# Performance work log

Hardware: AMD Instinct MI355X
Metric: run time of the kernel (lower is better)

Reference implementation:

```python
import jax, jax.numpy as jnp
import numpy as np

BN_EPS = 1e-5


def _bn(y, g, b, m, v):
    # BatchNorm1d in eval mode (running stats), faithful to torch's affine BN
    return (y - m) * jax.lax.rsqrt(v + BN_EPS) * g + b


def setup_inputs() -> dict:
    key = jax.random.key(0)
    ks = jax.random.split(key, 6)
    N, E, C_IN, C_OUT = 20000, 640000, 128, 256
    x = jax.random.normal(ks[0], (N, C_IN), dtype=jnp.float32)
    tpl_edge_index = jax.random.randint(ks[1], (2, E), 0, N, dtype=jnp.int64)
    def lin(k, o, i):
        return jax.random.normal(k, (o, i), dtype=jnp.float32) * 0.05
    inp = {
        'x': x,
        'tpl_edge_index': tpl_edge_index,
        'W1': lin(ks[2], C_OUT, 2 * C_IN), 'b1': jnp.zeros((C_OUT,), jnp.float32),
        'g1': jnp.ones((C_OUT,), jnp.float32), 'be1': jnp.zeros((C_OUT,), jnp.float32),
        'm1': jnp.zeros((C_OUT,), jnp.float32), 'v1': jnp.ones((C_OUT,), jnp.float32),
        'W2': lin(ks[3], C_OUT, C_OUT), 'b2': jnp.zeros((C_OUT,), jnp.float32),
        'g2': jnp.ones((C_OUT,), jnp.float32), 'be2': jnp.zeros((C_OUT,), jnp.float32),
        'm2': jnp.zeros((C_OUT,), jnp.float32), 'v2': jnp.ones((C_OUT,), jnp.float32),
        'W3': lin(ks[4], C_OUT, C_OUT), 'b3': jnp.zeros((C_OUT,), jnp.float32),
        'g3': jnp.ones((C_OUT,), jnp.float32), 'be3': jnp.zeros((C_OUT,), jnp.float32),
        'm3': jnp.zeros((C_OUT,), jnp.float32), 'v3': jnp.ones((C_OUT,), jnp.float32),
    }
    return inp


def reference(x, tpl_edge_index, W1, b1, g1, be1, m1, v1,
              W2, b2, g2, be2, m2, v2, W3, b3, g3, be3, m3, v3):
    N = x.shape[0]
    # remove_self_loops + add_self_loops: under max aggregation, duplicate
    # self-loop messages (x_j - x_i == 0) are idempotent, so appending one
    # self-loop per node is mathematically identical.
    loops = jnp.arange(N, dtype=tpl_edge_index.dtype)
    src = jnp.concatenate([tpl_edge_index[0], loops])  # x_j indices
    tgt = jnp.concatenate([tpl_edge_index[1], loops])  # x_i / aggregation indices
    x_i = x[tgt]                                       # [E+N, C_in]
    x_j = x[src]
    h = jnp.concatenate([x_i, x_j - x_i], axis=1)      # [E+N, 2*C_in]
    h = _bn(jax.nn.relu(h @ W1.T + b1), g1, be1, m1, v1)
    h = _bn(jax.nn.relu(h @ W2.T + b2), g2, be2, m2, v2)
    agg = jax.ops.segment_max(h, tgt, num_segments=N)  # scatter-max -> [N, C_out]
    out = _bn(jax.nn.relu(agg @ W3.T + b3), g3, be3, m3, v3)
    return out
```

## Files before the change

kernel.cpp:

```cpp
#include <hip/hip_runtime.h>
#include <stdint.h>

#define BN_EPS 1e-5f

typedef __bf16 bf16x8 __attribute__((ext_vector_type(8)));
typedef __bf16 bf16x2 __attribute__((ext_vector_type(2)));
typedef float  f32x4  __attribute__((ext_vector_type(4)));
typedef float  f32x2  __attribute__((ext_vector_type(2)));

__device__ __forceinline__ unsigned short f2bf(float f) {
    unsigned u = __float_as_uint(f);
    unsigned r = (u + 0x7FFFu + ((u >> 16) & 1u)) >> 16;
    return (unsigned short)r;
}
__device__ __forceinline__ unsigned pkb(float a, float b) {
    f32x2 f; f.x = a; f.y = b;
    bf16x2 h = __builtin_convertvector(f, bf16x2);
    return *(unsigned*)&h;
}
__device__ __forceinline__ unsigned ar2(unsigned p, unsigned q) {
    f32x2 a, b;
    a.x = __uint_as_float(p << 16);
    a.y = __uint_as_float(p & 0xFFFF0000u);
    b.x = __uint_as_float(q << 16);
    b.y = __uint_as_float(q & 0xFFFF0000u);
    f32x2 s = a + b;
    return pkb(fmaxf(s.x, 0.f), fmaxf(s.y, 0.f));
}
__device__ __forceinline__ int swz(int row, int k) {
    const int blk = k >> 3;
    const int sb = (blk & 24) | ((blk ^ row) & 7);
    return (row << 8) + (sb << 3) + (k & 7);
}
__device__ __forceinline__ int swz128(int row, int k) {
    const int blk = k >> 3;
    const int sb = (blk & 8) | ((blk ^ row) & 7);
    return (row << 7) + (sb << 3) + (k & 7);
}

__global__ void prep_kernel(
    const float* __restrict__ x, const int* __restrict__ eidx,
    int E, int M, int NX,
    const float* __restrict__ W1, const float* __restrict__ W2, const float* __restrict__ W3,
    const float* __restrict__ b1, const float* __restrict__ g1, const float* __restrict__ be1,
    const float* __restrict__ m1, const float* __restrict__ v1,
    const float* __restrict__ b2, const float* __restrict__ g2, const float* __restrict__ be2,
    const float* __restrict__ m2, const float* __restrict__ v2,
    const float* __restrict__ b3, const float* __restrict__ g3, const float* __restrict__ be3,
    const float* __restrict__ m3, const float* __restrict__ v3,
    unsigned short* __restrict__ W1b, unsigned short* __restrict__ W2b,
    unsigned short* __restrict__ W3b, float* __restrict__ consts,
    unsigned* __restrict__ mask2,
    unsigned short* __restrict__ xb, unsigned* __restrict__ count)
{
    const int idx = blockIdx.x * 256 + threadIdx.x;
    if (idx < 65536) {
        const int row = idx >> 8, c = idx & 255;
        float w1v = (c < 128) ? (W1[row * 256 + c] - W1[row * 256 + c + 128])
                              : W1[row * 256 + c];
        W1b[idx] = f2bf(w1v);
        const float s1c = g1[c] * rsqrtf(v1[c] + BN_EPS);
        W2b[idx] = f2bf(W2[idx] * s1c);
        const float s2c = g2[c] * rsqrtf(v2[c] + BN_EPS);
        W3b[idx] = f2bf(W3[idx] * s2c);
    }
    if (idx < 128) {
        const float sa = g2[2 * idx]     * rsqrtf(v2[2 * idx]     + BN_EPS);
        const float sb = g2[2 * idx + 1] * rsqrtf(v2[2 * idx + 1] + BN_EPS);
        mask2[idx] = (sa < 0.f ? 0xFFFFu : 0u) | ((sb < 0.f ? 0xFFFFu : 0u) << 16);
    }
    if (idx < 768) {
        const int l = idx >> 8, c = idx & 255;
        const float* bp  = l == 0 ? b1  : (l == 1 ? b2  : b3);
        const float* gp  = l == 0 ? g1  : (l == 1 ? g2  : g3);
        const float* bep = l == 0 ? be1 : (l == 1 ? be2 : be3);
        const float* mp  = l == 0 ? m1  : (l == 1 ? m2  : m3);
        const float* vp  = l == 0 ? v1  : (l == 1 ? v2  : v3);
        const float s = gp[c] * rsqrtf(vp[c] + BN_EPS);
        float bias = bp[c];
        if (l == 1) {
            float acc = 0.f;
            for (int k = 0; k < 256; k++) {
                const float s1k = g1[k] * rsqrtf(v1[k] + BN_EPS);
                acc += W2[c * 256 + k] * (be1[k] - m1[k] * s1k);
            }
            bias += acc;
        } else if (l == 2) {
            float acc = 0.f;
            for (int k = 0; k < 256; k++) {
                const float s2k = g2[k] * rsqrtf(v2[k] + BN_EPS);
                acc += W3[c * 256 + k] * (be2[k] - m2[k] * s2k);
            }
            bias += acc;
        }
        consts[l * 768 + c]       = bias;
        consts[l * 768 + 256 + c] = s;
        consts[l * 768 + 512 + c] = bep[c] - mp[c] * s;
    }
    if (idx < NX) xb[idx] = f2bf(x[idx]);
    if (idx < M) {
        const int tgt = (idx < E) ? eidx[E + idx] : (idx - E);
        atomicAdd(&count[tgt], 1u);
    }
}

__global__ __launch_bounds__(512) void pq_kernel(
    const unsigned short* __restrict__ xb, int N,
    const unsigned short* __restrict__ W1b,
    const float* __restrict__ consts,
    unsigned short* __restrict__ Pb, unsigned short* __restrict__ Qb)
{
    __shared__ unsigned short Xs[64 * 128];

    const int t = threadIdx.x;
    const int base = blockIdx.x * 64;

    {
        const int row = t >> 3, part = t & 7;
        const int node = base + row;
        const int c0 = part * 16;
        if (node < N) {
            const unsigned short* s = xb + (size_t)node * 128 + c0;
            *(uint4*)&Xs[swz128(row, c0)]     = *(const uint4*)(s);
            *(uint4*)&Xs[swz128(row, c0 + 8)] = *(const uint4*)(s + 8);
        } else {
            const uint4 z = {0u, 0u, 0u, 0u};
            *(uint4*)&Xs[swz128(row, c0)]     = z;
            *(uint4*)&Xs[swz128(row, c0 + 8)] = z;
        }
    }
    __syncthreads();

    const int lane = t & 63;
    const int wv   = t >> 6;
    const int n16  = lane & 15;
    const int qd   = lane >> 4;
    const int wc   = wv * 32;

    const f32x4 vzero = {0.f, 0.f, 0.f, 0.f};

    #pragma unroll
    for (int ph = 0; ph < 2; ph++) {
        f32x4 acc[2][4];
        #pragma unroll
        for (int i = 0; i < 2; i++)
            #pragma unroll
            for (int j = 0; j < 4; j++) acc[i][j] = vzero;

        #pragma unroll
        for (int ks = 0; ks < 4; ks++) {
            const int k0 = ks * 32 + qd * 8;
            bf16x8 a[2], b[4];
            #pragma unroll
            for (int ci = 0; ci < 2; ci++)
                a[ci] = *(const bf16x8*)&W1b[(size_t)(wc + ci * 16 + n16) * 256 + ph * 128 + k0];
            #pragma unroll
            for (int rj = 0; rj < 4; rj++)
                b[rj] = *(const bf16x8*)&Xs[swz128(rj * 16 + n16, k0)];
            #pragma unroll
            for (int ci = 0; ci < 2; ci++)
                #pragma unroll
                for (int rj = 0; rj < 4; rj++)
                    acc[ci][rj] = __builtin_amdgcn_mfma_f32_16x16x32_bf16(a[ci], b[rj], acc[ci][rj], 0, 0, 0);
        }

        unsigned short* dst = ph == 0 ? Pb : Qb;
        #pragma unroll
        for (int ci = 0; ci < 2; ci++) {
            const int col0 = wc + ci * 16 + qd * 4;
            float4 bb = {0.f, 0.f, 0.f, 0.f};
            if (ph == 0) bb = *(const float4*)&consts[col0];
            #pragma unroll
            for (int rj = 0; rj < 4; rj++) {
                const int node = base + rj * 16 + n16;
                if (node < N) {
                    uint2 p = {pkb(acc[ci][rj][0] + bb.x, acc[ci][rj][1] + bb.y),
                               pkb(acc[ci][rj][2] + bb.z, acc[ci][rj][3] + bb.w)};
                    *(uint2*)(dst + (size_t)node * 256 + col0) = p;
                }
            }
        }
    }
}

__global__ __launch_bounds__(1024) void scan_kernel(
    const unsigned* __restrict__ count, unsigned* __restrict__ cursor, int N)
{
    __shared__ unsigned part[1024];
    const int t = threadIdx.x;
    const int per = (N + 1023) / 1024;
    const int b = t * per;
    unsigned s = 0;
    for (int i = 0; i < per; i++) if (b + i < N) s += count[b + i];
    part[t] = s;
    __syncthreads();
    for (int off = 1; off < 1024; off <<= 1) {
        unsigned v = (t >= off) ? part[t - off] : 0u;
        __syncthreads();
        part[t] += v;
        __syncthreads();
    }
    unsigned run = (t > 0) ? part[t - 1] : 0u;
    for (int i = 0; i < per; i++) {
        if (b + i < N) {
            unsigned c = count[b + i];
            cursor[b + i] = run;
            run += c;
        }
    }
}

__global__ void scatter_kernel(const int* __restrict__ eidx, int E, int M,
                               unsigned* __restrict__ cursor, int* __restrict__ spair)
{
    const int i = blockIdx.x * 256 + threadIdx.x;
    if (i < M) {
        int s, tg;
        if (i < E) { s = eidx[i]; tg = eidx[E + i]; }
        else       { s = tg = i - E; }
        const unsigned pos = atomicAdd(&cursor[tg], 1u);
        int2* p = (int2*)spair;
        p[pos] = make_int2(s, tg);
    }
}

__global__ __launch_bounds__(512) void msg_kernel(
    const unsigned short* __restrict__ Pb,
    const unsigned short* __restrict__ Qb,
    const int* __restrict__ spair,
    int M,
    const unsigned short* __restrict__ W2b,
    const float* __restrict__ consts,
    const unsigned* __restrict__ mask2,
    unsigned* __restrict__ agg)
{
    __shared__ unsigned short At[64 * 256];
    __shared__ int tgt_l[64];

    const int t = threadIdx.x;
    const int base = blockIdx.x * 64;

    {
        const int row = t >> 3, part = t & 7;
        const int slot = base + row;
        const int c0 = part * 32;
        if (slot < M) {
            const int2 pr = *(const int2*)(spair + 2 * slot);
            if (part == 0) tgt_l[row] = pr.y;
            const unsigned short* Pp = Pb + (size_t)pr.y * 256 + c0;
            const unsigned short* Qp = Qb + (size_t)pr.x * 256 + c0;
            uint4 P4[4], Q4[4];
            #pragma unroll
            for (int w = 0; w < 4; w++) P4[w] = *(const uint4*)(Pp + w * 8);
            #pragma unroll
            for (int w = 0; w < 4; w++) Q4[w] = *(const uint4*)(Qp + w * 8);
            #pragma unroll
            for (int w = 0; w < 4; w++) {
                uint4 u;
                u.x = ar2(P4[w].x, Q4[w].x);
                u.y = ar2(P4[w].y, Q4[w].y);
                u.z = ar2(P4[w].z, Q4[w].z);
                u.w = ar2(P4[w].w, Q4[w].w);
                *(uint4*)&At[swz(row, c0 + w * 8)] = u;
            }
        } else {
            if (part == 0) tgt_l[row] = -1;
            const uint4 z = {0u, 0u, 0u, 0u};
            #pragma unroll
            for (int w = 0; w < 4; w++) *(uint4*)&At[swz(row, c0 + w * 8)] = z;
        }
    }
    __syncthreads();

    const int lane = t & 63;
    const int wv   = t >> 6;
    const int n16  = lane & 15;
    const int qd   = lane >> 4;
    const int wc   = wv * 32;

    const f32x4 vzero = {0.f, 0.f, 0.f, 0.f};
    f32x4 acc[2][4];
    #pragma unroll
    for (int i = 0; i < 2; i++)
        #pragma unroll
        for (int j = 0; j < 4; j++) acc[i][j] = vzero;

    #pragma unroll
    for (int ks = 0; ks < 8; ks++) {
        const int k0 = ks * 32 + qd * 8;
        bf16x8 a[2], b[4];
        #pragma unroll
        for (int ci = 0; ci < 2; ci++)
            a[ci] = *(const bf16x8*)&W2b[(size_t)(wc + ci * 16 + n16) * 256 + k0];
        #pragma unroll
        for (int rj = 0; rj < 4; rj++)
            b[rj] = *(const bf16x8*)&At[swz(rj * 16 + n16, k0)];
        #pragma unroll
        for (int ci = 0; ci < 2; ci++)
            #pragma unroll
            for (int rj = 0; rj < 4; rj++)
                acc[ci][rj] = __builtin_amdgcn_mfma_f32_16x16x32_bf16(a[ci], b[rj], acc[ci][rj], 0, 0, 0);
    }
    __syncthreads();

    {
        const float* B2 = consts + 768;
        #pragma unroll
        for (int ci = 0; ci < 2; ci++) {
            const int col0 = wc + ci * 16 + qd * 4;
            const float4 bb = *(const float4*)&B2[col0];
            const uint2 mk = *(const uint2*)&mask2[col0 >> 1];
            #pragma unroll
            for (int rj = 0; rj < 4; rj++) {
                const int row = rj * 16 + n16;
                float r0 = fmaxf(acc[ci][rj][0] + bb.x, 0.f);
                float r1 = fmaxf(acc[ci][rj][1] + bb.y, 0.f);
                float r2 = fmaxf(acc[ci][rj][2] + bb.z, 0.f);
                float r3 = fmaxf(acc[ci][rj][3] + bb.w, 0.f);
                uint2 p = {pkb(r0, r1) ^ mk.x, pkb(r2, r3) ^ mk.y};
                *(uint2*)&At[swz(row, col0)] = p;
            }
        }
    }
    __syncthreads();

    {
        const int r0 = (wv & 3) * 16;
        const int cb = (wv >> 2) * 128 + lane * 2;
        const int myt = (lane < 16) ? tgt_l[r0 + lane] : -1;
        int curT = -1;
        unsigned m0 = 0, m1 = 0;
        for (int r = 0; r < 16; r++) {
            const int tg = __shfl(myt, r);
            const unsigned k2 = *(const unsigned*)&At[swz(r0 + r, cb)];
            const unsigned k0 = k2 & 0xFFFFu, k1 = k2 >> 16;
            if (tg != curT) {
                if (curT >= 0) {
                    unsigned* p = &agg[(size_t)curT * 256 + cb];
                    atomicMax(p, m0); atomicMax(p + 1, m1);
                }
                curT = tg; m0 = k0; m1 = k1;
            } else {
                m0 = m0 > k0 ? m0 : k0;
                m1 = m1 > k1 ? m1 : k1;
            }
        }
        if (curT >= 0) {
            unsigned* p = &agg[(size_t)curT * 256 + cb];
            atomicMax(p, m0); atomicMax(p + 1, m1);
        }
    }
}

__global__ __launch_bounds__(256) void out_kernel(
    const unsigned* __restrict__ agg, int N,
    const unsigned short* __restrict__ W3b,
    const float* __restrict__ consts,
    const unsigned* __restrict__ mask2,
    float* __restrict__ out)
{
    __shared__ unsigned short At[32 * 256];

    const int t = threadIdx.x;
    const int base = blockIdx.x * 32;

    {
        const int row = t >> 3, part = t & 7;
        const int node = base + row;
        const int c0 = part * 32;
        if (node < N) {
            const unsigned* ap = agg + (size_t)node * 256 + c0;
            #pragma unroll
            for (int w = 0; w < 4; w++) {
                uint4 a = *(const uint4*)(ap + w * 8);
                uint4 b = *(const uint4*)(ap + w * 8 + 4);
                const uint4 mk = *(const uint4*)&mask2[(c0 + w * 8) >> 1];
                uint4 p;
                p.x = (a.x | (a.y << 16)) ^ mk.x;
                p.y = (a.z | (a.w << 16)) ^ mk.y;
                p.z = (b.x | (b.y << 16)) ^ mk.z;
                p.w = (b.z | (b.w << 16)) ^ mk.w;
                *(uint4*)&At[swz(row, c0 + w * 8)] = p;
            }
        } else {
            const uint4 z = {0u, 0u, 0u, 0u};
            #pragma unroll
            for (int w = 0; w < 4; w++) *(uint4*)&At[swz(row, c0 + w * 8)] = z;
        }
    }
    __syncthreads();

    const int lane = t & 63;
    const int wv   = t >> 6;
    const int n16  = lane & 15;
    const int qd   = lane >> 4;
    const int wc   = wv * 64;

    const f32x4 vzero = {0.f, 0.f, 0.f, 0.f};
    f32x4 acc[2][4];
    #pragma unroll
    for (int i = 0; i < 2; i++)
        #pragma unroll
        for (int j = 0; j < 4; j++) acc[i][j] = vzero;

    #pragma unroll
    for (int ks = 0; ks < 8; ks++) {
        const int k0 = ks * 32 + qd * 8;
        bf16x8 a[2];
        #pragma unroll
        for (int ri = 0; ri < 2; ri++)
            a[ri] = *(const bf16x8*)&At[swz(ri * 16 + n16, k0)];
        #pragma unroll
        for (int ci = 0; ci < 4; ci++) {
            bf16x8 b = *(const bf16x8*)&W3b[(size_t)(wc + ci * 16 + n16) * 256 + k0];
            #pragma unroll
            for (int ri = 0; ri < 2; ri++)
                acc[ri][ci] = __builtin_amdgcn_mfma_f32_16x16x32_bf16(a[ri], b, acc[ri][ci], 0, 0, 0);
        }
    }

    {
        const float* B3 = consts + 1536;
        const float* S3 = consts + 1536 + 256;
        const float* T3 = consts + 1536 + 512;
        #pragma unroll
        for (int ci = 0; ci < 4; ci++) {
            const int col = wc + ci * 16 + n16;
            const float bb = B3[col], ss = S3[col], tt = T3[col];
            #pragma unroll
            for (int ri = 0; ri < 2; ri++) {
                #pragma unroll
                for (int r = 0; r < 4; r++) {
                    const int row = ri * 16 + qd * 4 + r;
                    const int node = base + row;
                    if (node < N) {
                        float v = fmaxf(acc[ri][ci][r] + bb, 0.f) * ss + tt;
                        out[(size_t)node * 256 + col] = v;
                    }
                }
            }
        }
    }
}

extern "C" void kernel_launch(void* const* d_in, const int* in_sizes, int n_in,
                              void* d_out, int out_size, void* d_ws, size_t ws_size,
                              hipStream_t stream)
{
    const float* x  = (const float*)d_in[0];
    const int* eidx = (const int*)d_in[1];
    const int N = in_sizes[0] / 128;
    const int NX = in_sizes[0];
    const int E = in_sizes[1] / 2;
    const int M = E + N;

    char* ws = (char*)d_ws;
    unsigned short* W1b = (unsigned short*)(ws);
    unsigned short* W2b = (unsigned short*)(ws + 131072);
    unsigned short* W3b = (unsigned short*)(ws + 262144);
    float* consts       = (float*)(ws + 393216);
    unsigned* mask2     = (unsigned*)(ws + 402432);
    size_t off = 402944;
    unsigned short* xb  = (unsigned short*)(ws + off); off += (size_t)NX * 2;
    unsigned* agg       = (unsigned*)(ws + off);       off += (size_t)N * 256 * 4;
    unsigned* count     = (unsigned*)(ws + off);       off += (size_t)N * 4;
    unsigned* cursor    = (unsigned*)(ws + off);       off += (size_t)N * 4;
    int* spair          = (int*)(ws + off);            off += (size_t)M * 8;
    unsigned short* Pb  = (unsigned short*)(ws + off); off += (size_t)N * 256 * 2;
    unsigned short* Qb  = (unsigned short*)(ws + off);

    hipMemsetAsync(agg, 0, (size_t)N * 256 * 4, stream);
    hipMemsetAsync(count, 0, (size_t)N * 4, stream);

    int work = NX;
    if (M > work) work = M;
    if (65536 > work) work = 65536;
    hipLaunchKernelGGL(prep_kernel, dim3((work + 255) / 256), dim3(256), 0, stream,
        x, eidx, E, M, NX,
        (const float*)d_in[2], (const float*)d_in[8], (const float*)d_in[14],
        (const float*)d_in[3], (const float*)d_in[4], (const float*)d_in[5],
        (const float*)d_in[6], (const float*)d_in[7],
        (const float*)d_in[9], (const float*)d_in[10], (const float*)d_in[11],
        (const float*)d_in[12], (const float*)d_in[13],
        (const float*)d_in[15], (const float*)d_in[16], (const float*)d_in[17],
        (const float*)d_in[18], (const float*)d_in[19],
        W1b, W2b, W3b, consts, mask2, xb, count);

    hipLaunchKernelGGL(pq_kernel, dim3((N + 63) / 64), dim3(512), 0, stream,
        xb, N, W1b, consts, Pb, Qb);

    hipLaunchKernelGGL(scan_kernel, dim3(1), dim3(1024), 0, stream,
        count, cursor, N);
    hipLaunchKernelGGL(scatter_kernel, dim3((M + 255) / 256), dim3(256), 0, stream,
        eidx, E, M, cursor, spair);

    hipLaunchKernelGGL(msg_kernel, dim3((M + 63) / 64), dim3(512), 0, stream,
        Pb, Qb, spair, M, W2b, consts, mask2, agg);

    hipLaunchKernelGGL(out_kernel, dim3((N + 31) / 32), dim3(256), 0, stream,
        agg, N, W3b, consts, mask2, (float*)d_out);
}
```

Baseline: 490.9 us.

## Segmented max in registers in msg_kernel, fuse x bf16 conversion into pq_kernel

The msg_kernel epilogue no longer stages the activated tile through shared memory with two barriers. It now does a segmented max directly on MFMA accumulators in registers. Segment heads come from a ballot over sorted targets, and the reduction uses xor-shuffles before one atomicMax per segment and column. Separately, the fp32-to-bf16 conversion of x moves from prep_kernel into pq_kernel's load, which drops the xb buffer round trip, and scan_kernel's count sum is vectorised. The shuffle reduction adds ALU and shuffle work per segment, and the cost grows with the number of distinct targets per 64-row tile.

```diff
diff --git a/kernel.cpp b/kernel.cpp
--- a/kernel.cpp
+++ b/kernel.cpp
@@ -39,8 +39,8 @@
 }
 
 __global__ void prep_kernel(
-    const float* __restrict__ x, const int* __restrict__ eidx,
-    int E, int M, int NX,
+    const int* __restrict__ eidx,
+    int E, int M,
     const float* __restrict__ W1, const float* __restrict__ W2, const float* __restrict__ W3,
     const float* __restrict__ b1, const float* __restrict__ g1, const float* __restrict__ be1,
     const float* __restrict__ m1, const float* __restrict__ v1,
@@ -50,8 +50,7 @@
     const float* __restrict__ m3, const float* __restrict__ v3,
     unsigned short* __restrict__ W1b, unsigned short* __restrict__ W2b,
     unsigned short* __restrict__ W3b, float* __restrict__ consts,
-    unsigned* __restrict__ mask2,
-    unsigned short* __restrict__ xb, unsigned* __restrict__ count)
+    unsigned* __restrict__ mask2, unsigned* __restrict__ count)
 {
     const int idx = blockIdx.x * 256 + threadIdx.x;
     if (idx < 65536) {
@@ -97,7 +96,6 @@
         consts[l * 768 + 256 + c] = s;
         consts[l * 768 + 512 + c] = bep[c] - mp[c] * s;
     }
-    if (idx < NX) xb[idx] = f2bf(x[idx]);
     if (idx < M) {
         const int tgt = (idx < E) ? eidx[E + idx] : (idx - E);
         atomicAdd(&count[tgt], 1u);
@@ -105,7 +103,7 @@
 }
 
 __global__ __launch_bounds__(512) void pq_kernel(
-    const unsigned short* __restrict__ xb, int N,
+    const float* __restrict__ x, int N,
     const unsigned short* __restrict__ W1b,
     const float* __restrict__ consts,
     unsigned short* __restrict__ Pb, unsigned short* __restrict__ Qb)
@@ -120,9 +118,15 @@
         const int node = base + row;
         const int c0 = part * 16;
         if (node < N) {
-            const unsigned short* s = xb + (size_t)node * 128 + c0;
-            *(uint4*)&Xs[swz128(row, c0)]     = *(const uint4*)(s);
-            *(uint4*)&Xs[swz128(row, c0 + 8)] = *(const uint4*)(s + 8);
+            const float* s = x + (size_t)node * 128 + c0;
+            float4 a0 = *(const float4*)(s);
+            float4 a1 = *(const float4*)(s + 4);
+            float4 a2 = *(const float4*)(s + 8);
+            float4 a3 = *(const float4*)(s + 12);
+            uint4 p0 = {pkb(a0.x, a0.y), pkb(a0.z, a0.w), pkb(a1.x, a1.y), pkb(a1.z, a1.w)};
+            uint4 p1 = {pkb(a2.x, a2.y), pkb(a2.z, a2.w), pkb(a3.x, a3.y), pkb(a3.z, a3.w)};
+            *(uint4*)&Xs[swz128(row, c0)]     = p0;
+            *(uint4*)&Xs[swz128(row, c0 + 8)] = p1;
         } else {
             const uint4 z = {0u, 0u, 0u, 0u};
             *(uint4*)&Xs[swz128(row, c0)]     = z;
@@ -191,7 +195,14 @@
     const int per = (N + 1023) / 1024;
     const int b = t * per;
     unsigned s = 0;
-    for (int i = 0; i < per; i++) if (b + i < N) s += count[b + i];
+    if (b + per <= N && (per & 3) == 0) {
+        for (int i = 0; i < per; i += 4) {
+            uint4 c4 = *(const uint4*)(count + b + i);
+            s += c4.x + c4.y + c4.z + c4.w;
+        }
+    } else {
+        for (int i = 0; i < per; i++) if (b + i < N) s += count[b + i];
+    }
     part[t] = s;
     __syncthreads();
     for (int off = 1; off < 1024; off <<= 1) {
@@ -231,7 +242,6 @@
     int M,
     const unsigned short* __restrict__ W2b,
     const float* __restrict__ consts,
-    const unsigned* __restrict__ mask2,
     unsigned* __restrict__ agg)
 {
     __shared__ unsigned short At[64 * 256];
@@ -301,53 +311,64 @@
             for (int rj = 0; rj < 4; rj++)
                 acc[ci][rj] = __builtin_amdgcn_mfma_f32_16x16x32_bf16(a[ci], b[rj], acc[ci][rj], 0, 0, 0);
     }
-    __syncthreads();
-
-    {
-        const float* B2 = consts + 768;
-        #pragma unroll
-        for (int ci = 0; ci < 2; ci++) {
-            const int col0 = wc + ci * 16 + qd * 4;
-            const float4 bb = *(const float4*)&B2[col0];
-            const uint2 mk = *(const uint2*)&mask2[col0 >> 1];
-            #pragma unroll
-            for (int rj = 0; rj < 4; rj++) {
-                const int row = rj * 16 + n16;
-                float r0 = fmaxf(acc[ci][rj][0] + bb.x, 0.f);
-                float r1 = fmaxf(acc[ci][rj][1] + bb.y, 0.f);
-                float r2 = fmaxf(acc[ci][rj][2] + bb.z, 0.f);
-                float r3 = fmaxf(acc[ci][rj][3] + bb.w, 0.f);
-                uint2 p = {pkb(r0, r1) ^ mk.x, pkb(r2, r3) ^ mk.y};
-                *(uint2*)&At[swz(row, col0)] = p;
-            }
-        }
-    }
-    __syncthreads();
-
-    {
-        const int r0 = (wv & 3) * 16;
-        const int cb = (wv >> 2) * 128 + lane * 2;
-        const int myt = (lane < 16) ? tgt_l[r0 + lane] : -1;
-        int curT = -1;
-        unsigned m0 = 0, m1 = 0;
-        for (int r = 0; r < 16; r++) {
-            const int tg = __shfl(myt, r);
-            const unsigned k2 = *(const unsigned*)&At[swz(r0 + r, cb)];
-            const unsigned k0 = k2 & 0xFFFFu, k1 = k2 >> 16;
-            if (tg != curT) {
-                if (curT >= 0) {
-                    unsigned* p = &agg[(size_t)curT * 256 + cb];
-                    atomicMax(p, m0); atomicMax(p + 1, m1);
+
+    const int tgtRow = tgt_l[lane];
+    const int prevT  = __shfl_up(tgtRow, 1);
+    const bool head  = (lane == 0) || (tgtRow != prevT);
+    const unsigned long long hm = __ballot(head);
+
+    const float* B2 = consts + 768;
+    const float* S2 = consts + 768 + 256;
+    const float NEG = -3.0e38f;
+
+    #pragma unroll
+    for (int ci = 0; ci < 2; ci++) {
+        const int col0 = wc + ci * 16 + qd * 4;
+        const float4 bb = *(const float4*)&B2[col0];
+        const float4 s2 = *(const float4*)&S2[col0];
+        const bool f0 = s2.x < 0.f, f1 = s2.y < 0.f, f2 = s2.z < 0.f, f3 = s2.w < 0.f;
+        float u[4][4];
+        #pragma unroll
+        for (int rj = 0; rj < 4; rj++) {
+            float v0 = fmaxf(acc[ci][rj][0] + bb.x, 0.f);
+            float v1 = fmaxf(acc[ci][rj][1] + bb.y, 0.f);
+            float v2 = fmaxf(acc[ci][rj][2] + bb.z, 0.f);
+            float v3 = fmaxf(acc[ci][rj][3] + bb.w, 0.f);
+            u[0][rj] = f0 ? -v0 : v0;
+            u[1][rj] = f1 ? -v1 : v1;
+            u[2][rj] = f2 ? -v2 : v2;
+            u[3][rj] = f3 ? -v3 : v3;
+        }
+        unsigned long long rem = hm;
+        while (rem) {
+            const int a = (int)__builtin_ctzll(rem);
+            const unsigned long long rem2 = rem & (rem - 1);
+            const int bEnd = rem2 ? (int)__builtin_ctzll(rem2) : 64;
+            rem = rem2;
+            const int tg = __shfl(tgtRow, a);
+            float m[4];
+            #pragma unroll
+            for (int r = 0; r < 4; r++) {
+                float mm = NEG;
+                #pragma unroll
+                for (int rj = 0; rj < 4; rj++) {
+                    const int row = rj * 16 + n16;
+                    mm = fmaxf(mm, (row >= a && row < bEnd) ? u[r][rj] : NEG);
                 }
-                curT = tg; m0 = k0; m1 = k1;
-            } else {
-                m0 = m0 > k0 ? m0 : k0;
-                m1 = m1 > k1 ? m1 : k1;
-            }
-        }
-        if (curT >= 0) {
-            unsigned* p = &agg[(size_t)curT * 256 + cb];
-            atomicMax(p, m0); atomicMax(p + 1, m1);
+                m[r] = mm;
+            }
+            #pragma unroll
+            for (int d = 1; d < 16; d <<= 1)
+                #pragma unroll
+                for (int r = 0; r < 4; r++)
+                    m[r] = fmaxf(m[r], __shfl_xor(m[r], d));
+            if (tg >= 0 && n16 < 4) {
+                const int r = n16;
+                const bool fl = (r == 0) ? f0 : ((r == 1) ? f1 : ((r == 2) ? f2 : f3));
+                const float w = fl ? (0.f - m[r]) : m[r];
+                const unsigned key = (pkb(w, w) >> 16) ^ (fl ? 0xFFFFu : 0u);
+                atomicMax(&agg[(size_t)tg * 256 + col0 + r], key);
+            }
         }
     }
 }
@@ -450,7 +471,6 @@
     const float* x  = (const float*)d_in[0];
     const int* eidx = (const int*)d_in[1];
     const int N = in_sizes[0] / 128;
-    const int NX = in_sizes[0];
     const int E = in_sizes[1] / 2;
     const int M = E + N;
 
@@ -461,7 +481,6 @@
     float* consts       = (float*)(ws + 393216);
     unsigned* mask2     = (unsigned*)(ws + 402432);
     size_t off = 402944;
-    unsigned short* xb  = (unsigned short*)(ws + off); off += (size_t)NX * 2;
     unsigned* agg       = (unsigned*)(ws + off);       off += (size_t)N * 256 * 4;
     unsigned* count     = (unsigned*)(ws + off);       off += (size_t)N * 4;
     unsigned* cursor    = (unsigned*)(ws + off);       off += (size_t)N * 4;
@@ -472,11 +491,10 @@
     hipMemsetAsync(agg, 0, (size_t)N * 256 * 4, stream);
     hipMemsetAsync(count, 0, (size_t)N * 4, stream);
 
-    int work = NX;
-    if (M > work) work = M;
+    int work = M;
     if (65536 > work) work = 65536;
     hipLaunchKernelGGL(prep_kernel, dim3((work + 255) / 256), dim3(256), 0, stream,
-        x, eidx, E, M, NX,
+        eidx, E, M,
         (const float*)d_in[2], (const float*)d_in[8], (const float*)d_in[14],
         (const float*)d_in[3], (const float*)d_in[4], (const float*)d_in[5],
         (const float*)d_in[6], (const float*)d_in[7],
@@ -484,10 +502,10 @@
         (const float*)d_in[12], (const float*)d_in[13],
         (const float*)d_in[15], (const float*)d_in[16], (const float*)d_in[17],
         (const float*)d_in[18], (const float*)d_in[19],
-        W1b, W2b, W3b, consts, mask2, xb, count);
+        W1b, W2b, W3b, consts, mask2, count);
 
     hipLaunchKernelGGL(pq_kernel, dim3((N + 63) / 64), dim3(512), 0, stream,
-        xb, N, W1b, consts, Pb, Qb);
+        x, N, W1b, consts, Pb, Qb);
 
     hipLaunchKernelGGL(scan_kernel, dim3(1), dim3(1024), 0, stream,
         count, cursor, N);
@@ -495,7 +513,7 @@
         eidx, E, M, cursor, spair);
 
     hipLaunchKernelGGL(msg_kernel, dim3((M + 63) / 64), dim3(512), 0, stream,
-        Pb, Qb, spair, M, W2b, consts, mask2, agg);
+        Pb, Qb, spair, M, W2b, consts, agg);
 
     hipLaunchKernelGGL(out_kernel, dim3((N + 31) / 32), dim3(256), 0, stream,
         agg, N, W3b, consts, mask2, (float*)d_out);
```

New measurement: 519.7 us. 1.06x slower.
